# Optimization experiments

Measured on AMD Instinct MI355X. Metric: run time of the kernel, lower is better.

The kernel has to match this reference:

```python
import jax, jax.numpy as jnp
import numpy as np

B, N, C = 4, 1024, 1024
H = 16
HD = C // H
FF = 4 * C
EPS = 1e-6


def layernorm(x, g, b):
    mu = jnp.mean(x, axis=-1, keepdims=True)
    var = jnp.mean((x - mu) ** 2, axis=-1, keepdims=True)
    return (x - mu) * jax.lax.rsqrt(var + EPS) * g + b


def setup_inputs() -> dict:
    key = jax.random.key(0)
    ks = jax.random.split(key, 16)
    s = lambda fan_in: 1.0 / np.sqrt(fan_in)
    inp = {
        "x": jax.random.normal(ks[0], (B, N, C), dtype=jnp.float32),
        "qkv_w": jax.random.normal(ks[1], (3 * C, C), dtype=jnp.float32) * s(C),
        "qkv_b": jnp.zeros((3 * C,), jnp.float32),
        "attn_proj_w": jax.random.normal(ks[2], (C, C), dtype=jnp.float32) * s(C),
        "attn_proj_b": jnp.zeros((C,), jnp.float32),
        "blk_proj_w": jax.random.normal(ks[3], (C, C), dtype=jnp.float32) * s(C),
        "blk_proj_b": jnp.zeros((C,), jnp.float32),
        "ln1_g": jnp.ones((C,), jnp.float32),
        "ln1_b": jnp.zeros((C,), jnp.float32),
        "ln2_g": jnp.ones((C,), jnp.float32),
        "ln2_b": jnp.zeros((C,), jnp.float32),
        "fc1_w": jax.random.normal(ks[4], (FF, C), dtype=jnp.float32) * s(C),
        "fc1_b": jnp.zeros((FF,), jnp.float32),
        "fc2_w": jax.random.normal(ks[5], (C, FF), dtype=jnp.float32) * s(FF),
        "fc2_b": jnp.zeros((C,), jnp.float32),
        "mask": jnp.ones((B, N), jnp.int32),  # unused by the original forward
    }
    return inp


def reference(x, qkv_w, qkv_b, attn_proj_w, attn_proj_b, blk_proj_w, blk_proj_b,
              ln1_g, ln1_b, ln2_g, ln2_b, fc1_w, fc1_b, fc2_w, fc2_b, mask):
    shortcut = x
    xn = layernorm(x, ln1_g, ln1_b)

    # QKV projection: [B,N,3C] -> [3,B,H,N,HD]
    qkv = xn @ qkv_w.T + qkv_b
    qkv = qkv.reshape(B, N, 3, H, HD).transpose(2, 0, 3, 1, 4)
    q, k, v = qkv[0], qkv[1], qkv[2]
    scale = HD ** -0.5
    attn = jnp.einsum('bhqd,bhkd->bhqk', q * scale, k)
    attn = jax.nn.softmax(attn, axis=-1)
    o = jnp.einsum('bhqk,bhkd->bhqd', attn, v)
    o = o.transpose(0, 2, 1, 3).reshape(B, N, C)
    o = o @ attn_proj_w.T + attn_proj_b  # attention-internal proj

    x = shortcut + (o @ blk_proj_w.T + blk_proj_b)  # Block's extra proj + residual

    h = layernorm(x, ln2_g, ln2_b)
    h = jax.nn.gelu(h @ fc1_w.T + fc1_b, approximate=False)
    h = h @ fc2_w.T + fc2_b
    return x + h
```

## Files before the change

### kernel.cpp

```cpp
#include <hip/hip_runtime.h>

typedef unsigned short u16;
typedef __attribute__((ext_vector_type(8))) short short8;
typedef __attribute__((ext_vector_type(4))) float f32x4;

#define DEVI __device__ __forceinline__

static constexpr int Nn = 1024;
static constexpr int Cc = 1024;

DEVI u16 f2bf(float f) {
  union { float f; unsigned u; } v; v.f = f;
  unsigned r = v.u + 0x7fffu + ((v.u >> 16) & 1u);
  return (u16)(r >> 16);
}

DEVI void async_ld16(const void* g, void* lds) {
  __builtin_amdgcn_global_load_lds(
      (__attribute__((address_space(1))) void*)g,
      (__attribute__((address_space(3))) void*)lds, 16, 0, 0);
}

__global__ __launch_bounds__(256) void cvt_all(
    const float* __restrict__ s0, const float* __restrict__ s1,
    const float* __restrict__ s2, const float* __restrict__ s3,
    const float* __restrict__ s4, u16* __restrict__ out) {
  const size_t i = ((size_t)blockIdx.x * 256 + threadIdx.x) * 4;
  const float* src; size_t lo;
  if (i < 3145728)      { src = s0; lo = 0; }
  else if (i < 4194304) { src = s1; lo = 3145728; }
  else if (i < 5242880) { src = s2; lo = 4194304; }
  else if (i < 9437184) { src = s3; lo = 5242880; }
  else                  { src = s4; lo = 9437184; }
  const float4 v = *(const float4*)&src[i - lo];
  ushort4 o;
  o.x = f2bf(v.x); o.y = f2bf(v.y); o.z = f2bf(v.z); o.w = f2bf(v.w);
  *(ushort4*)&out[i] = o;
}

__global__ __launch_bounds__(256) void ln_bf16(const float* __restrict__ x,
                                               const float* __restrict__ gg,
                                               const float* __restrict__ bb,
                                               u16* __restrict__ out) {
  const int row = blockIdx.x;
  const float4 v = ((const float4*)(x + (size_t)row * 1024))[threadIdx.x];
  float s  = v.x + v.y + v.z + v.w;
  float s2 = v.x * v.x + v.y * v.y + v.z * v.z + v.w * v.w;
#pragma unroll
  for (int m = 1; m < 64; m <<= 1) { s += __shfl_xor(s, m); s2 += __shfl_xor(s2, m); }
  __shared__ float ps[4], ps2[4];
  const int wave = threadIdx.x >> 6;
  if ((threadIdx.x & 63) == 0) { ps[wave] = s; ps2[wave] = s2; }
  __syncthreads();
  s = ps[0] + ps[1] + ps[2] + ps[3];
  s2 = ps2[0] + ps2[1] + ps2[2] + ps2[3];
  const float mu = s * (1.0f / 1024.0f);
  const float var = s2 * (1.0f / 1024.0f) - mu * mu;
  const float rs = rsqrtf(var + 1e-6f);
  const float4 gv = ((const float4*)gg)[threadIdx.x];
  const float4 bv = ((const float4*)bb)[threadIdx.x];
  ushort4 o;
  o.x = f2bf((v.x - mu) * rs * gv.x + bv.x);
  o.y = f2bf((v.y - mu) * rs * gv.y + bv.y);
  o.z = f2bf((v.z - mu) * rs * gv.z + bv.z);
  o.w = f2bf((v.w - mu) * rs * gv.w + bv.w);
  ((ushort4*)(out + (size_t)row * 1024))[threadIdx.x] = o;
}

template <bool GELU_, bool OUTBF>
__global__ __launch_bounds__(512, 2) void gemm256(
    const u16* __restrict__ A, const u16* __restrict__ W,
    const float* __restrict__ bias, void* __restrict__ out,
    int M, int N, int K) {
  __shared__ __align__(16) u16 As[2][256 * 64];
  __shared__ __align__(16) u16 Bs[2][256 * 64];
  const int tid = threadIdx.x;
  const int wave = tid >> 6, lane = tid & 63;
  const int g = lane >> 4, lr = lane & 15;
  const int wm = wave >> 2, wn = wave & 3;
  const int ntile = N >> 8;
  const int nwg = gridDim.x;
  int bid = blockIdx.x;
  bid = (bid & 7) * (nwg >> 3) + (bid >> 3);
  const int brow = (bid / ntile) << 8, bcol = (bid % ntile) << 8;

  const int srow8 = lane >> 3;
  const int scg = (lane & 7) ^ srow8;
  const size_t aoff = (size_t)(brow + wave * 8 + srow8) * K + scg * 8;
  const size_t boff = (size_t)(bcol + wave * 8 + srow8) * K + scg * 8;
  const int ldst = wave * 1024;

  const int NT = K >> 6;

  f32x4 acc[8][4];
#pragma unroll
  for (int i = 0; i < 8; ++i)
#pragma unroll
    for (int j = 0; j < 4; ++j) acc[i][j] = (f32x4){0.f, 0.f, 0.f, 0.f};

  auto STA = [&](int s, int kt, int u) {
    async_ld16(A + aoff + (size_t)u * 64 * K + (size_t)kt * 64,
               (char*)&As[s][0] + u * 8192 + ldst);
  };
  auto STB = [&](int s, int kt, int u) {
    async_ld16(W + boff + (size_t)u * 64 * K + (size_t)kt * 64,
               (char*)&Bs[s][0] + u * 8192 + ldst);
  };

  const int aRdRow = (wm * 128 + lr) * 128;
  const int bRdRow = (wn * 64 + lr) * 128;
  const int swz = (lr & 7) << 4;

#pragma unroll
  for (int u = 0; u < 4; ++u) STB(0, 0, u);
#pragma unroll
  for (int u = 0; u < 4; ++u) STA(0, 0, u);
  asm volatile("s_waitcnt vmcnt(0)" ::: "memory");
  __builtin_amdgcn_s_barrier();

  for (int t = 0; t < NT; ++t) {
    const int c = t & 1, nc = c ^ 1;
    const int tn = (t + 1 < NT) ? t + 1 : t;
    const char* Ab = (const char*)&As[c][0];
    const char* Bb = (const char*)&Bs[c][0];

    short8 bf[4][2];
#pragma unroll
    for (int nf = 0; nf < 4; ++nf)
#pragma unroll
      for (int kk = 0; kk < 2; ++kk)
        bf[nf][kk] = *(const short8*)(Bb + bRdRow + nf * 2048 +
                                      ((kk * 64 + g * 16) ^ swz));
    short8 af[2][2];
#pragma unroll
    for (int mf = 0; mf < 2; ++mf)
#pragma unroll
      for (int kk = 0; kk < 2; ++kk)
        af[mf][kk] = *(const short8*)(Ab + aRdRow + mf * 2048 +
                                      ((kk * 64 + g * 16) ^ swz));
    STB(nc, tn, 0); STB(nc, tn, 1);
    __builtin_amdgcn_s_setprio(1);
#pragma unroll
    for (int mf = 0; mf < 2; ++mf)
#pragma unroll
      for (int nf = 0; nf < 4; ++nf)
#pragma unroll
        for (int kk = 0; kk < 2; ++kk)
          acc[mf][nf] = __builtin_amdgcn_mfma_f32_16x16x32_bf16(
              af[mf][kk], bf[nf][kk], acc[mf][nf], 0, 0, 0);
    __builtin_amdgcn_s_setprio(0);
    __builtin_amdgcn_s_barrier();

#pragma unroll
    for (int mf = 0; mf < 2; ++mf)
#pragma unroll
      for (int kk = 0; kk < 2; ++kk)
        af[mf][kk] = *(const short8*)(Ab + aRdRow + (mf + 2) * 2048 +
                                      ((kk * 64 + g * 16) ^ swz));
    STB(nc, tn, 2); STB(nc, tn, 3);
    __builtin_amdgcn_s_setprio(1);
#pragma unroll
    for (int mf = 0; mf < 2; ++mf)
#pragma unroll
      for (int nf = 0; nf < 4; ++nf)
#pragma unroll
        for (int kk = 0; kk < 2; ++kk)
          acc[mf + 2][nf] = __builtin_amdgcn_mfma_f32_16x16x32_bf16(
              af[mf][kk], bf[nf][kk], acc[mf + 2][nf], 0, 0, 0);
    __builtin_amdgcn_s_setprio(0);
    asm volatile("s_waitcnt vmcnt(4)" ::: "memory");
    __builtin_amdgcn_s_barrier();

#pragma unroll
    for (int mf = 0; mf < 2; ++mf)
#pragma unroll
      for (int kk = 0; kk < 2; ++kk)
        af[mf][kk] = *(const short8*)(Ab + aRdRow + (mf + 4) * 2048 +
                                      ((kk * 64 + g * 16) ^ swz));
    STA(nc, tn, 0); STA(nc, tn, 2);
    __builtin_amdgcn_s_setprio(1);
#pragma unroll
    for (int mf = 0; mf < 2; ++mf)
#pragma unroll
      for (int nf = 0; nf < 4; ++nf)
#pragma unroll
        for (int kk = 0; kk < 2; ++kk)
          acc[mf + 4][nf] = __builtin_amdgcn_mfma_f32_16x16x32_bf16(
              af[mf][kk], bf[nf][kk], acc[mf + 4][nf], 0, 0, 0);
    __builtin_amdgcn_s_setprio(0);
    __builtin_amdgcn_s_barrier();

#pragma unroll
    for (int mf = 0; mf < 2; ++mf)
#pragma unroll
      for (int kk = 0; kk < 2; ++kk)
        af[mf][kk] = *(const short8*)(Ab + aRdRow + (mf + 6) * 2048 +
                                      ((kk * 64 + g * 16) ^ swz));
    STA(nc, tn, 1); STA(nc, tn, 3);
    __builtin_amdgcn_s_setprio(1);
#pragma unroll
    for (int mf = 0; mf < 2; ++mf)
#pragma unroll
      for (int nf = 0; nf < 4; ++nf)
#pragma unroll
        for (int kk = 0; kk < 2; ++kk)
          acc[mf + 6][nf] = __builtin_amdgcn_mfma_f32_16x16x32_bf16(
              af[mf][kk], bf[nf][kk], acc[mf + 6][nf], 0, 0, 0);
    __builtin_amdgcn_s_setprio(0);
    asm volatile("s_waitcnt vmcnt(2)" ::: "memory");
    __builtin_amdgcn_s_barrier();
  }

#pragma unroll
  for (int mf = 0; mf < 8; ++mf)
#pragma unroll
    for (int nf = 0; nf < 4; ++nf) {
      const int cI = bcol + wn * 64 + nf * 16 + lr;
      const float bv = bias[cI];
#pragma unroll
      for (int reg = 0; reg < 4; ++reg) {
        const int r = brow + wm * 128 + mf * 16 + g * 4 + reg;
        float v = acc[mf][nf][reg] + bv;
        if (GELU_) v = 0.5f * v * (1.0f + erff(v * 0.70710678118654752f));
        if (OUTBF) ((u16*)out)[(size_t)r * N + cI] = f2bf(v);
        else       ((float*)out)[(size_t)r * N + cI] = v;
      }
    }
}

template <bool RESID, bool OUTBF>
__global__ __launch_bounds__(512, 2) void gemm128s(
    const u16* __restrict__ A, const u16* __restrict__ W,
    const float* __restrict__ bias, const float* __restrict__ resid,
    void* __restrict__ out, int M, int N, int K) {
  __shared__ __align__(16) u16 smem[32768];
  char* SA = (char*)smem;
  char* SB = SA + 32768;
  const int tid = threadIdx.x;
  const int wave = tid >> 6, lane = tid & 63;
  const int g = lane >> 4, lr = lane & 15;
  const int kg = wave & 1, ws = wave >> 1;
  const int wm = ws >> 1, wn = ws & 1;
  const int ntile = N >> 7;
  const int nwg = gridDim.x;
  int bid = blockIdx.x;
  bid = (bid & 7) * (nwg >> 3) + (bid >> 3);
  const int brow = (bid / ntile) << 7, bcol = (bid % ntile) << 7;

  const int sru = wave * 8 + (lane >> 3);
  const int scg = (lane & 7) ^ (lane >> 3);
  const int NT = K >> 6;

  f32x4 acc[4][4];
#pragma unroll
  for (int i = 0; i < 4; ++i)
#pragma unroll
    for (int j = 0; j < 4; ++j) acc[i][j] = (f32x4){0.f, 0.f, 0.f, 0.f};

  auto STA = [&](int s, int kt, int u) {
    async_ld16(A + (size_t)(brow + u * 64 + sru) * K + (size_t)kt * 64 + scg * 8,
               SA + s * 16384 + u * 8192 + wave * 1024);
  };
  auto STB = [&](int s, int kt, int u) {
    async_ld16(W + (size_t)(bcol + u * 64 + sru) * K + (size_t)kt * 64 + scg * 8,
               SB + s * 16384 + u * 8192 + wave * 1024);
  };

  const int colb = (kg * 64 + g * 16);
  const int swz = (lr & 7) << 4;

  STB(0, 0, 0); STB(0, 0, 1); STA(0, 0, 0); STA(0, 0, 1);
  asm volatile("s_waitcnt vmcnt(0)" ::: "memory");
  __builtin_amdgcn_s_barrier();

  for (int t = 0; t < NT; ++t) {
    const int c = t & 1, nc = c ^ 1;
    const int tn = (t + 1 < NT) ? t + 1 : t;
    const char* Ab = SA + c * 16384;
    const char* Bb = SB + c * 16384;

    short8 bf[4], af[2];
#pragma unroll
    for (int nf = 0; nf < 4; ++nf)
      bf[nf] = *(const short8*)(Bb + (wn * 64 + nf * 16 + lr) * 128 +
                                (colb ^ swz));
#pragma unroll
    for (int mf = 0; mf < 2; ++mf)
      af[mf] = *(const short8*)(Ab + (wm * 32 + mf * 16 + lr) * 128 +
                                (colb ^ swz));
    STB(nc, tn, 0); STB(nc, tn, 1);
    __builtin_amdgcn_s_setprio(1);
#pragma unroll
    for (int mf = 0; mf < 2; ++mf)
#pragma unroll
      for (int nf = 0; nf < 4; ++nf)
        acc[mf][nf] = __builtin_amdgcn_mfma_f32_16x16x32_bf16(
            af[mf], bf[nf], acc[mf][nf], 0, 0, 0);
    __builtin_amdgcn_s_setprio(0);
    asm volatile("s_waitcnt vmcnt(2)" ::: "memory");
    __builtin_amdgcn_s_barrier();

#pragma unroll
    for (int mf = 0; mf < 2; ++mf)
      af[mf] = *(const short8*)(Ab + (64 + wm * 32 + mf * 16 + lr) * 128 +
                                (colb ^ swz));
    STA(nc, tn, 0); STA(nc, tn, 1);
    __builtin_amdgcn_s_setprio(1);
#pragma unroll
    for (int mf = 0; mf < 2; ++mf)
#pragma unroll
      for (int nf = 0; nf < 4; ++nf)
        acc[mf + 2][nf] = __builtin_amdgcn_mfma_f32_16x16x32_bf16(
            af[mf], bf[nf], acc[mf + 2][nf], 0, 0, 0);
    __builtin_amdgcn_s_setprio(0);
    asm volatile("s_waitcnt vmcnt(1)" ::: "memory");
    __builtin_amdgcn_s_barrier();
  }

  asm volatile("s_waitcnt vmcnt(0)" ::: "memory");
  __syncthreads();
  float* pr = (float*)smem + (size_t)((wm << 1) | wn) * 4096;
  if (kg == 1) {
#pragma unroll
    for (int mf = 0; mf < 4; ++mf)
#pragma unroll
      for (int nf = 0; nf < 4; ++nf)
#pragma unroll
        for (int reg = 0; reg < 4; ++reg) {
          const int lrow = mf * 16 + g * 4 + reg;
          const int w = lrow * 64 +
                        ((nf * 16 + lr) ^ (g << 2) ^ ((g & 1) << 4));
          pr[w] = acc[mf][nf][reg];
        }
  }
  __syncthreads();
  if (kg == 0) {
#pragma unroll
    for (int mf = 0; mf < 4; ++mf) {
      const int rb = brow + ((mf < 2) ? wm * 32 + mf * 16
                                      : 64 + wm * 32 + (mf - 2) * 16);
#pragma unroll
      for (int nf = 0; nf < 4; ++nf) {
        const int cI = bcol + wn * 64 + nf * 16 + lr;
        const float bv = bias[cI];
#pragma unroll
        for (int reg = 0; reg < 4; ++reg) {
          const int lrow = mf * 16 + g * 4 + reg;
          const int w = lrow * 64 +
                        ((nf * 16 + lr) ^ (g << 2) ^ ((g & 1) << 4));
          const int r = rb + g * 4 + reg;
          float v = acc[mf][nf][reg] + pr[w] + bv;
          if (RESID) v += resid[(size_t)r * N + cI];
          if (OUTBF) ((u16*)out)[(size_t)r * N + cI] = f2bf(v);
          else       ((float*)out)[(size_t)r * N + cI] = v;
        }
      }
    }
  }
}

__global__ __launch_bounds__(256) void attn_kernel(const u16* __restrict__ qkv,
                                                   u16* __restrict__ o_out) {
  const int D = blockIdx.x;
  const int bh = (D & 7) + 8 * (D >> 7);
  const int qb = (D >> 3) & 15;
  const int b = bh >> 4, h = bh & 15;
  const int tid = threadIdx.x, wave = tid >> 6, lane = tid & 63;
  const int g = lane >> 4, lr = lane & 15;
  const u16* qg = qkv + (size_t)b * Nn * 3072 + h * 64;
  const u16* kg = qg + 1024;
  const u16* vg = qg + 2048;

  __shared__ __align__(16) u16 Kl[64 * 64];
  __shared__ __align__(16) u16 Vt[64 * 64];
  __shared__ __align__(16) u16 Pl[64 * 64];

  const int q0 = qb * 64 + wave * 16;
  short8 qf[2];
#pragma unroll
  for (int kf = 0; kf < 2; ++kf)
    qf[kf] = *(const short8*)(qg + (size_t)(q0 + lr) * 3072 + kf * 32 + g * 8);

  f32x4 o[4];
  float ll[4];
#pragma unroll
  for (int df = 0; df < 4; ++df) o[df] = (f32x4){0.f, 0.f, 0.f, 0.f};
#pragma unroll
  for (int r = 0; r < 4; ++r) ll[r] = 0.f;

  for (int t0 = 0; t0 < Nn; t0 += 64) {
#pragma unroll
    for (int r = 0; r < 2; ++r) {
      const int c = r * 256 + wave * 64 + lane;
      const int t = c >> 3;
      const int ob = ((c & 7) << 4) ^ ((t & 7) << 4);
      async_ld16(kg + (size_t)(t0 + t) * 3072 + (ob >> 1),
                 (char*)Kl + (size_t)(r * 256 + wave * 64) * 16);
    }
#pragma unroll
    for (int i = 0; i < 2; ++i) {
      const int idx = i * 256 + tid;
      const int d = idx & 63;
      const int tq = (idx >> 6) * 8;
      short8 vv;
#pragma unroll
      for (int j = 0; j < 8; ++j) vv[j] = (short)vg[(size_t)(t0 + tq + j) * 3072 + d];
      *(short8*)((char*)Vt + d * 128 + ((tq * 2) ^ ((d & 7) << 4))) = vv;
    }
    __syncthreads();

    short8 kfr[4][2];
#pragma unroll
    for (int tf = 0; tf < 4; ++tf) {
      const int t = tf * 16 + lr;
#pragma unroll
      for (int kf = 0; kf < 2; ++kf)
        kfr[tf][kf] = *(const short8*)((const char*)Kl + t * 128 +
                                       ((kf * 64 + g * 16) ^ ((t & 7) << 4)));
    }
    f32x4 s[4];
#pragma unroll
    for (int tf = 0; tf < 4; ++tf) {
      f32x4 z = (f32x4){0.f, 0.f, 0.f, 0.f};
      z = __builtin_amdgcn_mfma_f32_16x16x32_bf16(qf[0], kfr[tf][0], z, 0, 0, 0);
      z = __builtin_amdgcn_mfma_f32_16x16x32_bf16(qf[1], kfr[tf][1], z, 0, 0, 0);
      s[tf] = z;
    }

    short8 vfr[4][2];
#pragma unroll
    for (int df = 0; df < 4; ++df) {
      const int d = df * 16 + lr;
#pragma unroll
      for (int kf = 0; kf < 2; ++kf)
        vfr[df][kf] = *(const short8*)((const char*)Vt + d * 128 +
                                       ((kf * 64 + g * 16) ^ ((d & 7) << 4)));
    }

#pragma unroll
    for (int tf = 0; tf < 4; ++tf)
#pragma unroll
      for (int reg = 0; reg < 4; ++reg) {
        const float p = __expf(s[tf][reg] * 0.125f);
        s[tf][reg] = p;
        ll[reg] += p;
      }

#pragma unroll
    for (int tf = 0; tf < 4; ++tf)
#pragma unroll
      for (int reg = 0; reg < 4; ++reg) {
        const int m = wave * 16 + g * 4 + reg;
        const int t2 = (tf * 16 + lr) * 2;
        *(u16*)((char*)Pl + m * 128 + (t2 ^ ((m & 7) << 4))) = f2bf(s[tf][reg]);
      }
    short8 pa[2];
#pragma unroll
    for (int kf = 0; kf < 2; ++kf)
      pa[kf] = *(const short8*)((const char*)Pl + (wave * 16 + lr) * 128 +
                                ((kf * 64 + g * 16) ^ ((lr & 7) << 4)));
#pragma unroll
    for (int df = 0; df < 4; ++df) {
      o[df] = __builtin_amdgcn_mfma_f32_16x16x32_bf16(pa[0], vfr[df][0], o[df], 0, 0, 0);
      o[df] = __builtin_amdgcn_mfma_f32_16x16x32_bf16(pa[1], vfr[df][1], o[df], 0, 0, 0);
    }
    __syncthreads();
  }

#pragma unroll
  for (int reg = 0; reg < 4; ++reg) {
#pragma unroll
    for (int msk = 1; msk < 16; msk <<= 1) ll[reg] += __shfl_xor(ll[reg], msk);
    const float inv = 1.0f / ll[reg];
    const int row = b * Nn + qb * 64 + wave * 16 + g * 4 + reg;
#pragma unroll
    for (int df = 0; df < 4; ++df) {
      const int col = h * 64 + df * 16 + lr;
      o_out[(size_t)row * 1024 + col] = f2bf(o[df][reg] * inv);
    }
  }
}

extern "C" void kernel_launch(void* const* d_in, const int* in_sizes, int n_in,
                              void* d_out, int out_size, void* d_ws, size_t ws_size,
                              hipStream_t stream) {
  const float* x    = (const float*)d_in[0];
  const float* qkvw = (const float*)d_in[1];
  const float* qkvb = (const float*)d_in[2];
  const float* apw  = (const float*)d_in[3];
  const float* apb  = (const float*)d_in[4];
  const float* bpw  = (const float*)d_in[5];
  const float* bpb  = (const float*)d_in[6];
  const float* ln1g = (const float*)d_in[7];
  const float* ln1b = (const float*)d_in[8];
  const float* ln2g = (const float*)d_in[9];
  const float* ln2b = (const float*)d_in[10];
  const float* fc1w = (const float*)d_in[11];
  const float* fc1b = (const float*)d_in[12];
  const float* fc2w = (const float*)d_in[13];
  const float* fc2b = (const float*)d_in[14];
  float* out = (float*)d_out;

  char* ws = (char*)d_ws;
  size_t off = 0;
  auto alloc = [&](size_t bytes) {
    char* p = ws + off;
    off += (bytes + 255) & ~(size_t)255;
    return p;
  };
  u16* wqkv  = (u16*)alloc((size_t)3145728 * 2);
  u16* wap   = (u16*)alloc((size_t)1048576 * 2);
  u16* wbp   = (u16*)alloc((size_t)1048576 * 2);
  u16* wfc1  = (u16*)alloc((size_t)4194304 * 2);
  u16* wfc2  = (u16*)alloc((size_t)4194304 * 2);
  u16* xn    = (u16*)alloc((size_t)4194304 * 2);
  u16* qkvbf = (u16*)alloc((size_t)12582912 * 2);
  u16* obuf  = (u16*)alloc((size_t)4194304 * 2);
  u16* o2    = (u16*)alloc((size_t)4194304 * 2);
  float* x2  = (float*)alloc((size_t)4194304 * 4);
  u16* ff    = qkvbf;

  cvt_all<<<13312, 256, 0, stream>>>(qkvw, apw, bpw, fc1w, fc2w, wqkv);

  ln_bf16<<<4096, 256, 0, stream>>>(x, ln1g, ln1b, xn);

  gemm256<false, true><<<192, 512, 0, stream>>>(
      xn, wqkv, qkvb, qkvbf, 4096, 3072, 1024);

  attn_kernel<<<1024, 256, 0, stream>>>(qkvbf, obuf);

  gemm128s<false, true><<<256, 512, 0, stream>>>(
      obuf, wap, apb, nullptr, o2, 4096, 1024, 1024);

  gemm128s<true, false><<<256, 512, 0, stream>>>(
      o2, wbp, bpb, x, x2, 4096, 1024, 1024);

  ln_bf16<<<4096, 256, 0, stream>>>(x2, ln2g, ln2b, xn);

  gemm256<true, true><<<256, 512, 0, stream>>>(
      xn, wfc1, fc1b, ff, 4096, 4096, 1024);

  gemm128s<true, false><<<256, 512, 0, stream>>>(
      ff, wfc2, fc2b, x2, out, 4096, 1024, 4096);
}
```

Measured before the change: 240.7 us.

## Fold the two back-to-back projections into one weight and double-buffer attention K/V

Precomputes a combined weight Wc = Wbp·Wap (via a transposed bf16 copy of Wap and a small GEMM) and a combined bias cb = Wbp·apb + bpb, so the two chained 1024x1024 projections over 4096 tokens become a single GEMM. This removes one large GEMM and the intermediate o2 round trip, at the cost of extra per-call setup kernels (transpose, bias reduction, 1024^3 GEMM) and a change in bf16 rounding because the product is rounded once. The attention kernel also double-buffers K and V in LDS, prefetching the next tile during compute, and raises wave priority around the MFMA blocks.

```diff
diff --git a/kernel.cpp b/kernel.cpp
--- a/kernel.cpp
+++ b/kernel.cpp
@@ -36,6 +36,46 @@
   ushort4 o;
   o.x = f2bf(v.x); o.y = f2bf(v.y); o.z = f2bf(v.z); o.w = f2bf(v.w);
   *(ushort4*)&out[i] = o;
+}
+
+__global__ __launch_bounds__(256) void transpose_wT(const float* __restrict__ in,
+                                                    u16* __restrict__ out) {
+  __shared__ u16 tile[64][72];
+  const int bx = blockIdx.x & 15, by = blockIdx.x >> 4;
+  const int tr = threadIdx.x >> 2;
+  const int tc4 = (threadIdx.x & 3) * 16;
+#pragma unroll
+  for (int j = 0; j < 4; ++j) {
+    const float4 v = *(const float4*)&in[(size_t)(by * 64 + tr) * 1024 +
+                                         bx * 64 + tc4 + j * 4];
+    tile[tc4 + j * 4 + 0][tr] = f2bf(v.x);
+    tile[tc4 + j * 4 + 1][tr] = f2bf(v.y);
+    tile[tc4 + j * 4 + 2][tr] = f2bf(v.z);
+    tile[tc4 + j * 4 + 3][tr] = f2bf(v.w);
+  }
+  __syncthreads();
+#pragma unroll
+  for (int j = 0; j < 4; ++j) {
+    ushort4 o;
+    o.x = tile[tr][tc4 + j * 4 + 0];
+    o.y = tile[tr][tc4 + j * 4 + 1];
+    o.z = tile[tr][tc4 + j * 4 + 2];
+    o.w = tile[tr][tc4 + j * 4 + 3];
+    *(ushort4*)&out[(size_t)(bx * 64 + tr) * 1024 + by * 64 + tc4 + j * 4] = o;
+  }
+}
+
+__global__ __launch_bounds__(256) void cbias_k(const float* __restrict__ apb,
+                                               const float* __restrict__ bpw,
+                                               const float* __restrict__ bpb,
+                                               float* __restrict__ cb) {
+  const int j = blockIdx.x * 4 + (threadIdx.x >> 6);
+  const int lane = threadIdx.x & 63;
+  float s = 0.f;
+  for (int k = lane; k < 1024; k += 64) s += apb[k] * bpw[(size_t)j * 1024 + k];
+#pragma unroll
+  for (int m = 1; m < 64; m <<= 1) s += __shfl_xor(s, m);
+  if (lane == 0) cb[j] = s + bpb[j];
 }
 
 __global__ __launch_bounds__(256) void ln_bf16(const float* __restrict__ x,
@@ -371,8 +411,8 @@
   const u16* kg = qg + 1024;
   const u16* vg = qg + 2048;
 
-  __shared__ __align__(16) u16 Kl[64 * 64];
-  __shared__ __align__(16) u16 Vt[64 * 64];
+  __shared__ __align__(16) u16 Kl[2][64 * 64];
+  __shared__ __align__(16) u16 Vt[2][64 * 64];
   __shared__ __align__(16) u16 Pl[64 * 64];
 
   const int q0 = qb * 64 + wave * 16;
@@ -388,26 +428,47 @@
 #pragma unroll
   for (int r = 0; r < 4; ++r) ll[r] = 0.f;
 
-  for (int t0 = 0; t0 < Nn; t0 += 64) {
+  auto stageK = [&](int buf, int t0) {
 #pragma unroll
     for (int r = 0; r < 2; ++r) {
       const int c = r * 256 + wave * 64 + lane;
       const int t = c >> 3;
       const int ob = ((c & 7) << 4) ^ ((t & 7) << 4);
       async_ld16(kg + (size_t)(t0 + t) * 3072 + (ob >> 1),
-                 (char*)Kl + (size_t)(r * 256 + wave * 64) * 16);
-    }
+                 (char*)Kl[buf] + (size_t)(r * 256 + wave * 64) * 16);
+    }
+  };
+  const int vd = tid & 63;
+  const int vtq0 = (tid >> 6) * 8;
+  auto loadV = [&](short8* v, int t0) {
 #pragma unroll
     for (int i = 0; i < 2; ++i) {
-      const int idx = i * 256 + tid;
-      const int d = idx & 63;
-      const int tq = (idx >> 6) * 8;
-      short8 vv;
-#pragma unroll
-      for (int j = 0; j < 8; ++j) vv[j] = (short)vg[(size_t)(t0 + tq + j) * 3072 + d];
-      *(short8*)((char*)Vt + d * 128 + ((tq * 2) ^ ((d & 7) << 4))) = vv;
-    }
-    __syncthreads();
+      const int tq = vtq0 + i * 32;
+#pragma unroll
+      for (int j = 0; j < 8; ++j)
+        v[i][j] = (short)vg[(size_t)(t0 + tq + j) * 3072 + vd];
+    }
+  };
+  auto writeV = [&](int buf, short8* v) {
+#pragma unroll
+    for (int i = 0; i < 2; ++i) {
+      const int tq = vtq0 + i * 32;
+      *(short8*)((char*)Vt[buf] + vd * 128 + ((tq * 2) ^ ((vd & 7) << 4))) = v[i];
+    }
+  };
+
+  short8 vv[2];
+  stageK(0, 0);
+  loadV(vv, 0);
+  asm volatile("s_waitcnt vmcnt(0)" ::: "memory");
+  writeV(0, vv);
+  asm volatile("s_waitcnt lgkmcnt(0)" ::: "memory");
+  __builtin_amdgcn_s_barrier();
+
+  for (int t0 = 0; t0 < Nn; t0 += 64) {
+    const int c = (t0 >> 6) & 1, nc = c ^ 1;
+    const bool more = (t0 + 64 < Nn);
+    if (more) { stageK(nc, t0 + 64); loadV(vv, t0 + 64); }
 
     short8 kfr[4][2];
 #pragma unroll
@@ -415,10 +476,11 @@
       const int t = tf * 16 + lr;
 #pragma unroll
       for (int kf = 0; kf < 2; ++kf)
-        kfr[tf][kf] = *(const short8*)((const char*)Kl + t * 128 +
+        kfr[tf][kf] = *(const short8*)((const char*)Kl[c] + t * 128 +
                                        ((kf * 64 + g * 16) ^ ((t & 7) << 4)));
     }
     f32x4 s[4];
+    __builtin_amdgcn_s_setprio(1);
 #pragma unroll
     for (int tf = 0; tf < 4; ++tf) {
       f32x4 z = (f32x4){0.f, 0.f, 0.f, 0.f};
@@ -426,6 +488,7 @@
       z = __builtin_amdgcn_mfma_f32_16x16x32_bf16(qf[1], kfr[tf][1], z, 0, 0, 0);
       s[tf] = z;
     }
+    __builtin_amdgcn_s_setprio(0);
 
     short8 vfr[4][2];
 #pragma unroll
@@ -433,7 +496,7 @@
       const int d = df * 16 + lr;
 #pragma unroll
       for (int kf = 0; kf < 2; ++kf)
-        vfr[df][kf] = *(const short8*)((const char*)Vt + d * 128 +
+        vfr[df][kf] = *(const short8*)((const char*)Vt[c] + d * 128 +
                                        ((kf * 64 + g * 16) ^ ((d & 7) << 4)));
     }
 
@@ -459,12 +522,20 @@
     for (int kf = 0; kf < 2; ++kf)
       pa[kf] = *(const short8*)((const char*)Pl + (wave * 16 + lr) * 128 +
                                 ((kf * 64 + g * 16) ^ ((lr & 7) << 4)));
+    __builtin_amdgcn_s_setprio(1);
 #pragma unroll
     for (int df = 0; df < 4; ++df) {
       o[df] = __builtin_amdgcn_mfma_f32_16x16x32_bf16(pa[0], vfr[df][0], o[df], 0, 0, 0);
       o[df] = __builtin_amdgcn_mfma_f32_16x16x32_bf16(pa[1], vfr[df][1], o[df], 0, 0, 0);
     }
-    __syncthreads();
+    __builtin_amdgcn_s_setprio(0);
+
+    if (more) {
+      asm volatile("s_waitcnt vmcnt(0)" ::: "memory");
+      writeV(nc, vv);
+      asm volatile("s_waitcnt lgkmcnt(0)" ::: "memory");
+      __builtin_amdgcn_s_barrier();
+    }
   }
 
 #pragma unroll
@@ -516,11 +587,22 @@
   u16* xn    = (u16*)alloc((size_t)4194304 * 2);
   u16* qkvbf = (u16*)alloc((size_t)12582912 * 2);
   u16* obuf  = (u16*)alloc((size_t)4194304 * 2);
-  u16* o2    = (u16*)alloc((size_t)4194304 * 2);
   float* x2  = (float*)alloc((size_t)4194304 * 4);
+  u16* wapT  = (u16*)alloc((size_t)1048576 * 2);
+  u16* wc    = (u16*)alloc((size_t)1048576 * 2);
+  float* cb  = (float*)alloc(1024 * 4);
+  float* zb  = (float*)alloc(1024 * 4);
   u16* ff    = qkvbf;
+  (void)wap;
+
+  hipMemsetAsync(zb, 0, 1024 * 4, stream);
 
   cvt_all<<<13312, 256, 0, stream>>>(qkvw, apw, bpw, fc1w, fc2w, wqkv);
+  transpose_wT<<<256, 256, 0, stream>>>(apw, wapT);
+  cbias_k<<<256, 256, 0, stream>>>(apb, bpw, bpb, cb);
+
+  gemm128s<false, true><<<64, 512, 0, stream>>>(
+      wbp, wapT, zb, nullptr, wc, 1024, 1024, 1024);
 
   ln_bf16<<<4096, 256, 0, stream>>>(x, ln1g, ln1b, xn);
 
@@ -529,11 +611,8 @@
 
   attn_kernel<<<1024, 256, 0, stream>>>(qkvbf, obuf);
 
-  gemm128s<false, true><<<256, 512, 0, stream>>>(
-      obuf, wap, apb, nullptr, o2, 4096, 1024, 1024);
-
   gemm128s<true, false><<<256, 512, 0, stream>>>(
-      o2, wbp, bpb, x, x2, 4096, 1024, 1024);
+      obuf, wc, cb, x, x2, 4096, 1024, 1024);
 
   ln_bf16<<<4096, 256, 0, stream>>>(x2, ln2g, ln2b, xn);
 
```

After: 262.9 us. 9.2% more time.
